# Kernel tuning notes

Measured on AMD Instinct MI355X. Metric: run time of the kernel, lower is better.

The kernel has to match this reference:

```python
import jax, jax.numpy as jnp
import numpy as np

B, L, C, H, W = 1, 16, 16, 128, 256  # L = T_chunk = K_chunk (single chunk, causal)
DECAY = 0.1  # decay_val


def setup_inputs() -> dict:
    key = jax.random.key(0)
    k1, k2 = jax.random.split(key)
    img = jax.random.normal(k1, (B, L, C, H, W), jnp.float32)
    # flows in normalized [-1,1] grid units; keep displacements modest
    cum_flow = jax.random.normal(k2, (B, L, 2, H, W), jnp.float32) * 0.1
    t = jnp.arange(L)
    mask = (t[:, None] >= t[None, :]).astype(jnp.float32)          # causal [T,K]
    decay_dist = jnp.abs(t[:, None] - t[None, :]).astype(jnp.float32)  # [T,K]
    return {"img": img, "cum_flow": cum_flow, "mask": mask, "decay_dist": decay_dist}


def _bilinear_sample(img, gx, gy):
    # img: [B,K,C,H,W]; gx, gy: [B,K,H,W] in normalized [-1,1] coords.
    # x wraps around (periodic), y clamps -- matching the kernel's index handling.
    ix = (gx + 1.0) * (W * 0.5) - 0.5
    iy = (gy + 1.0) * (H * 0.5) - 0.5
    x0 = jnp.floor(ix)
    y0 = jnp.floor(iy)
    wx = ix - x0  # fractional weights
    wy = iy - y0
    x0i = x0.astype(jnp.int32)
    y0i = y0.astype(jnp.int32)
    x0r = jnp.mod(x0i, W)
    x1r = jnpp = jnp.mod(x0i + 1, W)
    y0c = jnp.clip(y0i, 0, H - 1)
    y1c = jnp.clip(y0i + 1, 0, H - 1)

    K = img.shape[1]
    imgf = img.reshape(B, K, C, H * W)

    def gather(yy, xx):
        idx = (yy * W + xx).reshape(B, K, 1, H * W)  # broadcast over C
        return jnp.take_along_axis(imgf, idx, axis=-1).reshape(B, K, C, H, W)

    va = gather(y0c, x0r)  # (y0, x0)
    vb = gather(y1c, x0r)  # (y1, x0)
    vc = gather(y0c, x1r)  # (y0, x1)
    vd = gather(y1c, x1r)  # (y1, x1)
    wx_ = wx[:, :, None]   # [B,K,1,H,W]
    wy_ = wy[:, :, None]
    return (va * (1.0 - wx_) * (1.0 - wy_) + vb * (1.0 - wx_) * wy_
            + vc * wx_ * (1.0 - wy_) + vd * wx_ * wy_)


def reference(img, cum_flow, mask, decay_dist):
    # base grid (align_corners=False style pixel centers)
    base_x = (jnp.arange(W, dtype=jnp.float32) * (2.0 / W) - 1.0 + 1.0 / W)[None, None, :]  # [1,1,W]
    base_y = (jnp.arange(H, dtype=jnp.float32) * (2.0 / H) - 1.0 + 1.0 / H)[None, :, None]  # [1,H,1]

    weights = mask * jnp.exp(-DECAY * decay_dist)  # [T,K] decay-weighted causal mask
    fx = cum_flow[:, :, 0]  # [B,L,H,W]
    fy = cum_flow[:, :, 1]

    def step(carry, inp):
        ft_x, ft_y, w_row = inp  # ft_*: [B,H,W]; w_row: [K]
        gx = base_x[None] + (ft_x[:, None] - fx)  # [B,K,H,W]
        gy = base_y[None] + (ft_y[:, None] - fy)
        gx = jnp.mod(gx + 1.0, 2.0) - 1.0          # wrap x into [-1,1)
        sampled = _bilinear_sample(img, gx, gy)    # [B,K,C,H,W]
        out_t = jnp.einsum('k,bkchw->bchw', w_row, sampled)
        return carry, out_t

    xs = (jnp.moveaxis(fx, 1, 0), jnp.moveaxis(fy, 1, 0), weights)  # over t
    _, outs = jax.lax.scan(step, 0.0, xs)          # [T,B,C,H,W]
    return jnp.moveaxis(outs, 0, 1)                # [B,T,C,H,W]
```

## Files before the change

### kernel.cpp

```cpp
#include <hip/hip_runtime.h>

constexpr int Lc = 16;
constexpr int Cc = 16;
constexpr int Hc = 128;
constexpr int Wc = 256;
constexpr float DECAYc = 0.1f;
constexpr int HWc = Hc * Wc;

__device__ inline unsigned short f2bf(float f) {
    unsigned int u = __float_as_uint(f);
    u += 0x7fffu + ((u >> 16) & 1u);
    return (unsigned short)(u >> 16);
}
__device__ inline float2 bf2f2(unsigned int u) {
    return make_float2(__uint_as_float(u << 16),
                       __uint_as_float(u & 0xffff0000u));
}

constexpr int topbit(unsigned m) { int r = 0; while (m >>= 1) ++r; return r; }

__global__ __launch_bounds__(256) void transpose_cvt_bf16(
    const float* __restrict__ img, unsigned short* __restrict__ imgTb)
{
    const int tid = threadIdx.x;
    const int h2 = tid & 1;
    const int wq = tid >> 1;
    const int kf  = blockIdx.x >> 5;
    const int px0 = (blockIdx.x & 31) * 1024;
    const float* __restrict__ srcb = img + (size_t)kf * Cc * HWc + (size_t)(8 * h2) * HWc;
#pragma unroll
    for (int rr = 0; rr < 8; ++rr) {
        const int px = px0 + rr * 128 + wq;
        float v[8];
#pragma unroll
        for (int c = 0; c < 8; ++c) v[c] = srcb[c * HWc + px];
        uint4 o;
        o.x = (unsigned int)f2bf(v[0]) | ((unsigned int)f2bf(v[1]) << 16);
        o.y = (unsigned int)f2bf(v[2]) | ((unsigned int)f2bf(v[3]) << 16);
        o.z = (unsigned int)f2bf(v[4]) | ((unsigned int)f2bf(v[5]) << 16);
        o.w = (unsigned int)f2bf(v[6]) | ((unsigned int)f2bf(v[7]) << 16);
        *(uint4*)(imgTb + ((size_t)kf * HWc + px) * Cc + 8 * h2) = o;
    }
}

template <unsigned MASK, int TLO, int THI>
__device__ __forceinline__ void do_chunk_m(
    int k, const unsigned short* __restrict__ bk, int q,
    const float* sx1, const float* sy1, float fxk, float fyk,
    const float* __restrict__ wtab, float4* acc)
{
    constexpr int NT = THI - TLO + 1;
    int   offs[NT][4];
    float wts [NT][4];
    uint2 ld  [NT][4];

#pragma unroll
    for (int t = TLO; t <= THI; ++t) {
        if (!((MASK >> t) & 1u)) continue;
        if (t > k) {
            const int j = t - TLO;
            const float wkt = wtab[t * Lc + k];
            const float ix = (sx1[t] - fxk) * (Wc * 0.5f) - 0.5f;
            const float iy = (sy1[t] - fyk) * (Hc * 0.5f) - 0.5f;
            const float x0f = floorf(ix);
            const float y0f = floorf(iy);
            const float wx = ix - x0f;
            const float wy = iy - y0f;
            const int x0 = (int)x0f;
            const int y0 = (int)y0f;
            const int x0r = x0 & (Wc - 1);
            const int x1r = (x0 + 1) & (Wc - 1);
            const int y0c = min(max(y0, 0), Hc - 1);
            const int y1c = min(max(y0 + 1, 0), Hc - 1);
            const float wb = wkt * wy;
            const float wa = wkt - wb;
            const float omx = 1.0f - wx;
            wts[j][0] = wa * omx;
            wts[j][1] = wa * wx;
            wts[j][2] = wb * omx;
            wts[j][3] = wb * wx;
            offs[j][0] = y0c * Wc + x0r;
            offs[j][1] = y0c * Wc + x1r;
            offs[j][2] = y1c * Wc + x0r;
            offs[j][3] = y1c * Wc + x1r;
        }
    }
#pragma unroll
    for (int t = TLO; t <= THI; ++t) {
        if (!((MASK >> t) & 1u)) continue;
        if (t > k) {
            const int j = t - TLO;
#pragma unroll
            for (int n = 0; n < 4; ++n)
                ld[j][n] = ((const uint2*)(bk + (size_t)offs[j][n] * Cc))[q];
        }
    }
#pragma unroll
    for (int t = TLO; t <= THI; ++t) {
        if (!((MASK >> t) & 1u)) continue;
        if (t > k) {
            const int j = t - TLO;
#pragma unroll
            for (int n = 0; n < 4; ++n) {
                const float2 f01 = bf2f2(ld[j][n].x);
                const float2 f23 = bf2f2(ld[j][n].y);
                const float a = wts[j][n];
                acc[t].x += a * f01.x;
                acc[t].y += a * f01.y;
                acc[t].z += a * f23.x;
                acc[t].w += a * f23.y;
            }
        }
    }
}

template <unsigned MASK>
__device__ __forceinline__ void run_quarter(
    const unsigned short* __restrict__ imgTb,
    const float* __restrict__ cum_flow,
    const float* __restrict__ img,
    float* __restrict__ out,
    const float* wtab,
    int q, int pix, float base_x, float base_y)
{
    constexpr unsigned LOOPM = MASK & ~1u;

    float sx1[Lc], sy1[Lc];
#pragma unroll
    for (int t = 0; t < Lc; ++t) {
        if (!((LOOPM >> t) & 1u)) continue;
        sx1[t] = base_x + cum_flow[(t * 2 + 0) * HWc + pix] + 1.0f;
        sy1[t] = base_y + cum_flow[(t * 2 + 1) * HWc + pix] + 1.0f;
    }

    float4 acc[Lc];
#pragma unroll
    for (int t = 0; t < Lc; ++t)
        if ((MASK >> t) & 1u) acc[t] = make_float4(0.f, 0.f, 0.f, 0.f);

    constexpr int KMAX = topbit(MASK);
    for (int k = 0; k < KMAX; ++k) {
        const float fxk = cum_flow[(k * 2 + 0) * HWc + pix];
        const float fyk = cum_flow[(k * 2 + 1) * HWc + pix];
        const unsigned short* __restrict__ bk = imgTb + (size_t)k * HWc * Cc;
        do_chunk_m<LOOPM, 1, 7>(k, bk, q, sx1, sy1, fxk, fyk, wtab, acc);
        do_chunk_m<LOOPM, 8, 15>(k, bk, q, sx1, sy1, fxk, fyk, wtab, acc);
    }

#pragma unroll
    for (int t = 0; t < Lc; ++t) {
        if (!((MASK >> t) & 1u)) continue;
        const float* __restrict__ ip = img + ((size_t)t * Cc + 4 * q) * HWc + pix;
        float* __restrict__ op = out + ((size_t)t * Cc + 4 * q) * HWc + pix;
        op[0 * HWc] = acc[t].x + ip[0 * HWc];
        op[1 * HWc] = acc[t].y + ip[1 * HWc];
        op[2 * HWc] = acc[t].z + ip[2 * HWc];
        op[3 * HWc] = acc[t].w + ip[3 * HWc];
    }
}

__global__ __launch_bounds__(256, 6) void gridsample_bf16_wq(
    const unsigned short* __restrict__ imgTb,
    const float* __restrict__ cum_flow,
    const float* __restrict__ mask,
    const float* __restrict__ decay,
    const float* __restrict__ img,
    float* __restrict__ out)
{
    __shared__ float wtab[Lc * Lc];
    const int tid = threadIdx.x;
    if (tid < Lc * Lc)
        wtab[tid] = mask[tid] * __expf(-DECAYc * decay[tid]);
    __syncthreads();

    const int q    = tid & 3;
    const int px16 = (tid >> 2) & 15;
    const int wv   = tid >> 6;
    const int b    = blockIdx.x;
    const int band = b & 7;
    const int sub  = b >> 3;
    const int h = band * 16 + (sub >> 4);
    const int w = (sub & 15) * 16 + px16;
    const int pix = h * Wc + w;

    const float base_x = w * (2.0f / Wc) - 1.0f + 1.0f / Wc;
    const float base_y = h * (2.0f / Hc) - 1.0f + 1.0f / Hc;

    switch (wv) {
        case 0:  run_quarter<0x8240u>(imgTb, cum_flow, img, out, wtab, q, pix, base_x, base_y); break;
        case 1:  run_quarter<0x5010u>(imgTb, cum_flow, img, out, wtab, q, pix, base_x, base_y); break;
        case 2:  run_quarter<0x280Eu>(imgTb, cum_flow, img, out, wtab, q, pix, base_x, base_y); break;
        default: run_quarter<0x05A1u>(imgTb, cum_flow, img, out, wtab, q, pix, base_x, base_y); break;
    }
}

__global__ __launch_bounds__(256) void gridsample_warp_acc(
    const float* __restrict__ img, const float* __restrict__ cum_flow,
    const float* __restrict__ mask, const float* __restrict__ decay,
    float* __restrict__ out)
{
    const int w = threadIdx.x, h = blockIdx.x, t = blockIdx.y;
    const int pix = h * Wc + w;
    const float base_x = w * (2.0f / Wc) - 1.0f + 1.0f / Wc;
    const float base_y = h * (2.0f / Hc) - 1.0f + 1.0f / Hc;
    const float fxt = cum_flow[(t * 2 + 0) * HWc + pix];
    const float fyt = cum_flow[(t * 2 + 1) * HWc + pix];
    float acc[Cc];
#pragma unroll
    for (int c = 0; c < Cc; ++c) acc[c] = 0.0f;
    for (int k = 0; k <= t; ++k) {
        const float wkt = mask[t * Lc + k] * __expf(-DECAYc * decay[t * Lc + k]);
        const float fxk = cum_flow[(k * 2 + 0) * HWc + pix];
        const float fyk = cum_flow[(k * 2 + 1) * HWc + pix];
        float gx = base_x + (fxt - fxk);
        const float gy = base_y + (fyt - fyk);
        float m = gx + 1.0f;
        m -= 2.0f * floorf(m * 0.5f);
        gx = m - 1.0f;
        const float ix = (gx + 1.0f) * (Wc * 0.5f) - 0.5f;
        const float iy = (gy + 1.0f) * (Hc * 0.5f) - 0.5f;
        const float x0f = floorf(ix), y0f = floorf(iy);
        const float wx = ix - x0f, wy = iy - y0f;
        const int x0 = (int)x0f, y0 = (int)y0f;
        const int x0r = x0 & (Wc - 1), x1r = (x0 + 1) & (Wc - 1);
        const int y0c = min(max(y0, 0), Hc - 1), y1c = min(max(y0 + 1, 0), Hc - 1);
        const float a00 = wkt * (1.0f - wx) * (1.0f - wy);
        const float a01 = wkt * (1.0f - wx) * wy;
        const float a10 = wkt * wx * (1.0f - wy);
        const float a11 = wkt * wx * wy;
        const int o00 = y0c * Wc + x0r, o01 = y1c * Wc + x0r;
        const int o10 = y0c * Wc + x1r, o11 = y1c * Wc + x1r;
        const float* __restrict__ ik = img + (size_t)k * Cc * HWc;
#pragma unroll
        for (int c = 0; c < Cc; ++c) {
            const float* __restrict__ p = ik + c * HWc;
            acc[c] += p[o00] * a00 + p[o01] * a01 + p[o10] * a10 + p[o11] * a11;
        }
    }
    float* __restrict__ op = out + (size_t)t * Cc * HWc + pix;
#pragma unroll
    for (int c = 0; c < Cc; ++c) op[c * HWc] = acc[c];
}

extern "C" void kernel_launch(void* const* d_in, const int* in_sizes, int n_in,
                              void* d_out, int out_size, void* d_ws, size_t ws_size,
                              hipStream_t stream) {
    const float* img      = (const float*)d_in[0];
    const float* cum_flow = (const float*)d_in[1];
    const float* mask     = (const float*)d_in[2];
    const float* decay    = (const float*)d_in[3];
    float* out = (float*)d_out;

    const size_t needed = (size_t)Lc * HWc * Cc * sizeof(unsigned short);
    if (ws_size >= needed) {
        unsigned short* imgTb = (unsigned short*)d_ws;
        transpose_cvt_bf16<<<dim3(512), 256, 0, stream>>>(img, imgTb);
        gridsample_bf16_wq<<<dim3(2048), 256, 0, stream>>>(
            imgTb, cum_flow, mask, decay, img, out);
    } else {
        dim3 grid(Hc, Lc, 1);
        gridsample_warp_acc<<<grid, Wc, 0, stream>>>(img, cum_flow, mask, decay, out);
    }
}
```

Measured before the change: 171.2 us.

## Split channels in halves per thread with 16-byte bf16 gathers

Each thread now handles 8 channels (half of C) per pixel instead of 4, so each bilinear tap is one 16-byte load instead of an 8-byte load. Two threads now cover a pixel instead of four, which halves the redundant coordinate and weight computation per pixel. Blocks cover 32 pixels, the grid is halved, and the per-wave time-step masks are rebalanced. Accumulator registers double, so launch bounds drop to 4 waves per SIMD, trading occupancy and latency hiding for fewer, wider loads.

Measured after the change: 162.6 us. -5.0%, faster.

```diff
diff --git a/kernel.cpp b/kernel.cpp
--- a/kernel.cpp
+++ b/kernel.cpp
@@ -44,15 +44,15 @@
 }
 
 template <unsigned MASK, int TLO, int THI>
-__device__ __forceinline__ void do_chunk_m(
-    int k, const unsigned short* __restrict__ bk, int q,
+__device__ __forceinline__ void do_chunk16(
+    int k, const unsigned short* __restrict__ bk, int half,
     const float* sx1, const float* sy1, float fxk, float fyk,
-    const float* __restrict__ wtab, float4* acc)
+    const float* __restrict__ wtab, float (*acc)[8])
 {
     constexpr int NT = THI - TLO + 1;
     int   offs[NT][4];
     float wts [NT][4];
-    uint2 ld  [NT][4];
+    uint4 ld  [NT][4];
 
 #pragma unroll
     for (int t = TLO; t <= THI; ++t) {
@@ -92,7 +92,7 @@
             const int j = t - TLO;
 #pragma unroll
             for (int n = 0; n < 4; ++n)
-                ld[j][n] = ((const uint2*)(bk + (size_t)offs[j][n] * Cc))[q];
+                ld[j][n] = ((const uint4*)(bk + (size_t)offs[j][n] * Cc))[half];
         }
     }
 #pragma unroll
@@ -102,13 +102,19 @@
             const int j = t - TLO;
 #pragma unroll
             for (int n = 0; n < 4; ++n) {
+                const float a = wts[j][n];
                 const float2 f01 = bf2f2(ld[j][n].x);
                 const float2 f23 = bf2f2(ld[j][n].y);
-                const float a = wts[j][n];
-                acc[t].x += a * f01.x;
-                acc[t].y += a * f01.y;
-                acc[t].z += a * f23.x;
-                acc[t].w += a * f23.y;
+                const float2 f45 = bf2f2(ld[j][n].z);
+                const float2 f67 = bf2f2(ld[j][n].w);
+                acc[t][0] += a * f01.x;
+                acc[t][1] += a * f01.y;
+                acc[t][2] += a * f23.x;
+                acc[t][3] += a * f23.y;
+                acc[t][4] += a * f45.x;
+                acc[t][5] += a * f45.y;
+                acc[t][6] += a * f67.x;
+                acc[t][7] += a * f67.y;
             }
         }
     }
@@ -121,7 +127,7 @@
     const float* __restrict__ img,
     float* __restrict__ out,
     const float* wtab,
-    int q, int pix, float base_x, float base_y)
+    int half, int pix, float base_x, float base_y)
 {
     constexpr unsigned LOOPM = MASK & ~1u;
 
@@ -133,33 +139,35 @@
         sy1[t] = base_y + cum_flow[(t * 2 + 1) * HWc + pix] + 1.0f;
     }
 
-    float4 acc[Lc];
-#pragma unroll
-    for (int t = 0; t < Lc; ++t)
-        if ((MASK >> t) & 1u) acc[t] = make_float4(0.f, 0.f, 0.f, 0.f);
+    float acc[Lc][8];
+#pragma unroll
+    for (int t = 0; t < Lc; ++t) {
+        if (!((MASK >> t) & 1u)) continue;
+#pragma unroll
+        for (int c = 0; c < 8; ++c) acc[t][c] = 0.f;
+    }
 
     constexpr int KMAX = topbit(MASK);
     for (int k = 0; k < KMAX; ++k) {
         const float fxk = cum_flow[(k * 2 + 0) * HWc + pix];
         const float fyk = cum_flow[(k * 2 + 1) * HWc + pix];
         const unsigned short* __restrict__ bk = imgTb + (size_t)k * HWc * Cc;
-        do_chunk_m<LOOPM, 1, 7>(k, bk, q, sx1, sy1, fxk, fyk, wtab, acc);
-        do_chunk_m<LOOPM, 8, 15>(k, bk, q, sx1, sy1, fxk, fyk, wtab, acc);
+        do_chunk16<LOOPM, 1, 7>(k, bk, half, sx1, sy1, fxk, fyk, wtab, acc);
+        do_chunk16<LOOPM, 8, 15>(k, bk, half, sx1, sy1, fxk, fyk, wtab, acc);
     }
 
 #pragma unroll
     for (int t = 0; t < Lc; ++t) {
         if (!((MASK >> t) & 1u)) continue;
-        const float* __restrict__ ip = img + ((size_t)t * Cc + 4 * q) * HWc + pix;
-        float* __restrict__ op = out + ((size_t)t * Cc + 4 * q) * HWc + pix;
-        op[0 * HWc] = acc[t].x + ip[0 * HWc];
-        op[1 * HWc] = acc[t].y + ip[1 * HWc];
-        op[2 * HWc] = acc[t].z + ip[2 * HWc];
-        op[3 * HWc] = acc[t].w + ip[3 * HWc];
-    }
-}
-
-__global__ __launch_bounds__(256, 6) void gridsample_bf16_wq(
+        const float* __restrict__ ip = img + ((size_t)t * Cc + 8 * half) * HWc + pix;
+        float* __restrict__ op = out + ((size_t)t * Cc + 8 * half) * HWc + pix;
+#pragma unroll
+        for (int c = 0; c < 8; ++c)
+            op[c * HWc] = acc[t][c] + ip[c * HWc];
+    }
+}
+
+__global__ __launch_bounds__(256, 4) void gridsample_bf16_h16(
     const unsigned short* __restrict__ imgTb,
     const float* __restrict__ cum_flow,
     const float* __restrict__ mask,
@@ -173,24 +181,24 @@
         wtab[tid] = mask[tid] * __expf(-DECAYc * decay[tid]);
     __syncthreads();
 
-    const int q    = tid & 3;
-    const int px16 = (tid >> 2) & 15;
+    const int half = tid & 1;
+    const int px32 = (tid >> 1) & 31;
     const int wv   = tid >> 6;
     const int b    = blockIdx.x;
     const int band = b & 7;
     const int sub  = b >> 3;
-    const int h = band * 16 + (sub >> 4);
-    const int w = (sub & 15) * 16 + px16;
+    const int h = band * 16 + (sub >> 3);
+    const int w = (sub & 7) * 32 + px32;
     const int pix = h * Wc + w;
 
     const float base_x = w * (2.0f / Wc) - 1.0f + 1.0f / Wc;
     const float base_y = h * (2.0f / Hc) - 1.0f + 1.0f / Hc;
 
     switch (wv) {
-        case 0:  run_quarter<0x8240u>(imgTb, cum_flow, img, out, wtab, q, pix, base_x, base_y); break;
-        case 1:  run_quarter<0x5010u>(imgTb, cum_flow, img, out, wtab, q, pix, base_x, base_y); break;
-        case 2:  run_quarter<0x280Eu>(imgTb, cum_flow, img, out, wtab, q, pix, base_x, base_y); break;
-        default: run_quarter<0x05A1u>(imgTb, cum_flow, img, out, wtab, q, pix, base_x, base_y); break;
+        case 0:  run_quarter<0x8124u>(imgTb, cum_flow, img, out, wtab, half, pix, base_x, base_y); break;
+        case 1:  run_quarter<0x4242u>(imgTb, cum_flow, img, out, wtab, half, pix, base_x, base_y); break;
+        case 2:  run_quarter<0x2418u>(imgTb, cum_flow, img, out, wtab, half, pix, base_x, base_y); break;
+        default: run_quarter<0x1881u>(imgTb, cum_flow, img, out, wtab, half, pix, base_x, base_y); break;
     }
 }
 
@@ -255,7 +263,7 @@
     if (ws_size >= needed) {
         unsigned short* imgTb = (unsigned short*)d_ws;
         transpose_cvt_bf16<<<dim3(512), 256, 0, stream>>>(img, imgTb);
-        gridsample_bf16_wq<<<dim3(2048), 256, 0, stream>>>(
+        gridsample_bf16_h16<<<dim3(1024), 256, 0, stream>>>(
             imgTb, cum_flow, mask, decay, img, out);
     } else {
         dim3 grid(Hc, Lc, 1);
```
